# Performance work log

Hardware: AMD Instinct MI355X
Metric: run time of the kernel (lower is better)

Reference implementation:

```python
import jax, jax.numpy as jnp
import numpy as np

B, S, D_MODEL, N_HEADS, HIDDEN = 4, 2048, 1024, 16, 4096
D_HEAD = D_MODEL // N_HEADS
LN_EPS = 1e-5


def setup_inputs() -> dict:
    key = jax.random.key(0)
    ks = jax.random.split(key, 20)
    s = 0.02
    return {
        "X": jax.random.normal(ks[0], (B, S, D_MODEL), dtype=jnp.float32),
        # attention projections (stored [in, out]; y = x @ W + b)
        "Wq": jax.random.normal(ks[1], (D_MODEL, D_MODEL), dtype=jnp.float32) * s,
        "bq": jnp.zeros((D_MODEL,), jnp.float32),
        "Wk": jax.random.normal(ks[2], (D_MODEL, D_MODEL), dtype=jnp.float32) * s,
        "bk": jnp.zeros((D_MODEL,), jnp.float32),
        "Wv": jax.random.normal(ks[3], (D_MODEL, D_MODEL), dtype=jnp.float32) * s,
        "bv": jnp.zeros((D_MODEL,), jnp.float32),
        "Wo": jax.random.normal(ks[4], (D_MODEL, D_MODEL), dtype=jnp.float32) * s,
        "bo": jnp.zeros((D_MODEL,), jnp.float32),
        # layernorm 1
        "g1": jnp.ones((D_MODEL,), jnp.float32),
        "beta1": jnp.zeros((D_MODEL,), jnp.float32),
        # FFN
        "W1": jax.random.normal(ks[5], (D_MODEL, HIDDEN), dtype=jnp.float32) * s,
        "b1": jnp.zeros((HIDDEN,), jnp.float32),
        "W2": jax.random.normal(ks[6], (HIDDEN, D_MODEL), dtype=jnp.float32) * s,
        "b2": jnp.zeros((D_MODEL,), jnp.float32),
        # layernorm 2
        "g2": jnp.ones((D_MODEL,), jnp.float32),
        "beta2": jnp.zeros((D_MODEL,), jnp.float32),
    }


def _layer_norm(x, gamma, beta):
    mu = jnp.mean(x, axis=-1, keepdims=True)
    var = jnp.mean(jnp.square(x - mu), axis=-1, keepdims=True)
    return (x - mu) * jax.lax.rsqrt(var + LN_EPS) * gamma + beta


def reference(X, Wq, bq, Wk, bk, Wv, bv, Wo, bo, g1, beta1, W1, b1, W2, b2, g2, beta2):
    b, s, d = X.shape
    # multi-head attention (dropout is identity in eval mode)
    q = (X @ Wq + bq).reshape(b, s, N_HEADS, D_HEAD)
    k = (X @ Wk + bk).reshape(b, s, N_HEADS, D_HEAD)
    v = (X @ Wv + bv).reshape(b, s, N_HEADS, D_HEAD)
    scale = 1.0 / np.sqrt(D_HEAD).astype(np.float32)
    scores = jnp.einsum('bqhd,bkhd->bhqk', q, k) * scale
    attn = jax.nn.softmax(scores, axis=-1)
    ctx = jnp.einsum('bhqk,bkhd->bqhd', attn, v).reshape(b, s, d)
    attn_out = ctx @ Wo + bo
    # AddNorm 1
    Y = _layer_norm(X + attn_out, g1, beta1)
    # FFN
    ffn_out = jax.nn.relu(Y @ W1 + b1) @ W2 + b2
    # AddNorm 2
    return _layer_norm(Y + ffn_out, g2, beta2)
```

## Files before the change

### kernel.cpp

```cpp
#include <hip/hip_runtime.h>
#include <stdint.h>

typedef unsigned short u16;
typedef short bf16x8 __attribute__((ext_vector_type(8)));
typedef float f32x4 __attribute__((ext_vector_type(4)));
typedef float f32x16 __attribute__((ext_vector_type(16)));
typedef u16 u16x4 __attribute__((ext_vector_type(4)));
typedef u16 u16x8 __attribute__((ext_vector_type(8)));

#define LOG2E 1.4426950408889634f
#define QSCALE (0.125f * LOG2E)

__device__ __forceinline__ u16 f2bf(float f) {
  union { float f; uint32_t u; } x; x.f = f;
  uint32_t r = x.u + 0x7fffu + ((x.u >> 16) & 1u);
  return (u16)(r >> 16);
}
__device__ __forceinline__ u16 f2bf_ru(float f) {
  union { float f; uint32_t u; } x; x.f = f;
  return (u16)((x.u + 0x8000u) >> 16);
}
__device__ __forceinline__ float bf2f(u16 h) {
  union { uint32_t u; float f; } x; x.u = ((uint32_t)h) << 16;
  return x.f;
}
__device__ __forceinline__ uint32_t cvtpk(float lo, float hi) {
  uint32_t r;
  asm("v_cvt_pk_bf16_f32 %0, %1, %2" : "=v"(r) : "v"(lo), "v"(hi));
  return r;
}
__device__ __forceinline__ int swz3(int row) { return (row ^ (row >> 3)) & 7; }

__device__ __forceinline__ void gload_lds16(const void* g, void* lds) {
  __builtin_amdgcn_global_load_lds(
      (const __attribute__((address_space(1))) void*)g,
      (__attribute__((address_space(3))) void*)lds, 16, 0, 0);
}

__global__ __launch_bounds__(256) void cast_bf16(const float* __restrict__ in,
                                                 u16* __restrict__ out, int n8) {
  int i = blockIdx.x * 256 + threadIdx.x;
  const int stride = gridDim.x * 256;
  for (; i < n8; i += stride) {
    const f32x4* p = (const f32x4*)in + (size_t)i * 2;
    f32x4 a = p[0], b = p[1];
    u16x8 o;
    o[0] = f2bf(a[0]); o[1] = f2bf(a[1]); o[2] = f2bf(a[2]); o[3] = f2bf(a[3]);
    o[4] = f2bf(b[0]); o[5] = f2bf(b[1]); o[6] = f2bf(b[2]); o[7] = f2bf(b[3]);
    ((u16x8*)out)[i] = o;
  }
}

__global__ __launch_bounds__(256) void concat3(const float* __restrict__ a,
                                               const float* __restrict__ b,
                                               const float* __restrict__ c,
                                               float* __restrict__ o) {
  int i = blockIdx.x * 256 + threadIdx.x;
  if (i < 3072)
    o[i] = i < 1024 ? a[i] * QSCALE : (i < 2048 ? b[i - 1024] : c[i - 2048]);
}

__global__ __launch_bounds__(256) void transpose_cast(const float* __restrict__ in,
                                                      u16* __restrict__ out, int R, int C,
                                                      float scale) {
  __shared__ float tile[32][33];
  const int bc = blockIdx.x * 32, br = blockIdx.y * 32;
  const int tx = threadIdx.x & 31, ty = threadIdx.x >> 5;
#pragma unroll
  for (int i = 0; i < 32; i += 8)
    tile[ty + i][tx] = in[(size_t)(br + ty + i) * C + bc + tx];
  __syncthreads();
#pragma unroll
  for (int i = 0; i < 32; i += 8)
    out[(size_t)(bc + ty + i) * R + br + tx] = f2bf(tile[tx][ty + i] * scale);
}

__global__ __launch_bounds__(256) void vtrans(const u16* __restrict__ QKV,
                                              u16* __restrict__ Vtg) {
  __shared__ u16 tl[64][65];
  const int t = threadIdx.x;
  const int sblk = blockIdx.x, h = blockIdx.y, b = blockIdx.z;
  const int s0 = sblk * 64;
  const size_t ibase = ((size_t)b * 2048) * 3072 + 2048 + h * 64;
#pragma unroll
  for (int i = 0; i < 2; i++) {
    const int idx = i * 256 + t;
    const int sl = idx >> 3, d0 = (idx & 7) * 8;
    bf16x8 v = *(const bf16x8*)&QKV[ibase + (size_t)(s0 + sl) * 3072 + d0];
#pragma unroll
    for (int e = 0; e < 8; e++) tl[d0 + e][sl] = (u16)v[e];
  }
  __syncthreads();
  const size_t ob = ((size_t)(b * 16 + h) * 64) * 2048;
#pragma unroll
  for (int i = 0; i < 2; i++) {
    const int idx = i * 256 + t;
    const int r = idx >> 3, c0 = (idx & 7) * 8;
    u16x8 o;
#pragma unroll
    for (int e = 0; e < 8; e++) o[e] = tl[r][c0 + e];
    *(u16x8*)&Vtg[ob + (size_t)r * 2048 + s0 + c0] = o;
  }
}

template <int RELU>
__global__ __launch_bounds__(512, 2) void gemm8p(const u16* __restrict__ A,
                                                 const u16* __restrict__ BT,
                                                 const float* __restrict__ bias,
                                                 u16* __restrict__ Cb,
                                                 int M, int N, int K, int nbx) {
  __shared__ u16 As[2][256 * 64];
  __shared__ u16 Bs[2][256 * 64];
  const int t = threadIdx.x;
  const int w = t >> 6, lane = t & 63;
  const int l5 = lane & 31, hf = lane >> 5;
  const int wr = w >> 2, wc = w & 3;
  int bid = (int)blockIdx.x;
  const int cpx = (int)gridDim.x >> 3;
  bid = (bid & 7) * cpx + (bid >> 3);
  const int m0 = (bid / nbx) * 256, n0 = (bid % nbx) * 256;
  const int NT = K >> 6;
  const int row64 = t >> 3;
  const int colp = ((t & 7) ^ swz3(row64)) << 3;

#define STG_A(buf, tile, q) \
  gload_lds16(A + (size_t)(m0 + (q)*64 + row64) * K + ((tile) << 6) + colp, \
              &As[buf][(q)*4096 + w * 512])
#define STG_B(buf, tile, q) \
  gload_lds16(BT + (size_t)(n0 + (q)*64 + row64) * K + ((tile) << 6) + colp, \
              &Bs[buf][(q)*4096 + w * 512])
#define LDA32(dst, mfi, kb) { const int r_ = wr * 128 + (mfi)*32 + l5; \
  dst = *(const bf16x8*)&As[cur][r_ * 64 + (((((kb) << 1) + hf) ^ swz3(r_)) << 3)]; }
#define LDB32(dst, nfi, kb) { const int r_ = wc * 64 + (nfi)*32 + l5; \
  dst = *(const bf16x8*)&Bs[cur][r_ * 64 + (((((kb) << 1) + hf) ^ swz3(r_)) << 3)]; }
#define MFMA32(mh, nfi, barr) \
  __builtin_amdgcn_s_setprio(1); \
  _Pragma("unroll") for (int kb = 0; kb < 4; kb++) \
  _Pragma("unroll") for (int i = 0; i < 2; i++) \
    acc[((mh)*2 + i) * 2 + (nfi)] = __builtin_amdgcn_mfma_f32_32x32x16_bf16( \
        af[i][kb], barr[kb], acc[((mh)*2 + i) * 2 + (nfi)], 0, 0, 0); \
  __builtin_amdgcn_s_setprio(0);
#define BAR1() __builtin_amdgcn_s_barrier(); \
  asm volatile("s_waitcnt lgkmcnt(0)" ::: "memory"); \
  __builtin_amdgcn_sched_barrier(0)

  f32x16 acc[8];
#pragma unroll
  for (int i = 0; i < 8; i++)
#pragma unroll
    for (int j = 0; j < 16; j++) acc[i][j] = 0.f;

  STG_A(0, 0, 0); STG_A(0, 0, 2);
  STG_B(0, 0, 0); STG_B(0, 0, 1); STG_B(0, 0, 2); STG_B(0, 0, 3);
  STG_A(0, 0, 1); STG_A(0, 0, 3);
  asm volatile("s_waitcnt vmcnt(2)" ::: "memory");
  __builtin_amdgcn_s_barrier();

  for (int tile = 0; tile < NT; ++tile) {
    const int cur = tile & 1, nxt = cur ^ 1;
    const bool hn = (tile + 1) < NT;
    bf16x8 af[2][4], b0[4], b1[4];
#pragma unroll
    for (int kb = 0; kb < 4; kb++) { LDA32(af[0][kb], 0, kb); LDA32(af[1][kb], 1, kb); }
#pragma unroll
    for (int kb = 0; kb < 4; kb++) { LDB32(b0[kb], 0, kb); }
    if (hn) { STG_A(nxt, tile + 1, 0); STG_A(nxt, tile + 1, 2); }
    BAR1();
    MFMA32(0, 0, b0);
    __builtin_amdgcn_s_barrier();
#pragma unroll
    for (int kb = 0; kb < 4; kb++) { LDB32(b1[kb], 1, kb); }
    if (hn) { STG_B(nxt, tile + 1, 0); STG_B(nxt, tile + 1, 1); }
    BAR1();
    MFMA32(0, 1, b1);
    if (hn) { asm volatile("s_waitcnt vmcnt(4)" ::: "memory"); }
    else    { asm volatile("s_waitcnt vmcnt(0)" ::: "memory"); }
    __builtin_amdgcn_s_barrier();
#pragma unroll
    for (int kb = 0; kb < 4; kb++) { LDA32(af[0][kb], 2, kb); LDA32(af[1][kb], 3, kb); }
    if (hn) { STG_B(nxt, tile + 1, 2); STG_B(nxt, tile + 1, 3); }
    BAR1();
    MFMA32(1, 0, b0);
    __builtin_amdgcn_s_barrier();
    if (hn) { STG_A(nxt, tile + 1, 1); STG_A(nxt, tile + 1, 3); }
    BAR1();
    MFMA32(1, 1, b1);
    if (hn) { asm volatile("s_waitcnt vmcnt(2)" ::: "memory"); }
    __builtin_amdgcn_s_barrier();
  }
#undef STG_A
#undef STG_B
#undef LDA32
#undef LDB32
#undef MFMA32
#undef BAR1

#pragma unroll
  for (int mf = 0; mf < 4; mf++) {
#pragma unroll
    for (int nf = 0; nf < 2; nf++) {
      const int c = n0 + wc * 64 + nf * 32 + l5;
      const float bv = bias[c];
#pragma unroll
      for (int reg = 0; reg < 16; reg++) {
        const int r = m0 + wr * 128 + mf * 32 + (reg & 3) + 8 * (reg >> 2) + 4 * hf;
        float v = acc[mf * 2 + nf][reg] + bv;
        if (RELU) v = fmaxf(v, 0.f);
        Cb[(size_t)r * N + c] = f2bf(v);
      }
    }
  }
}

template <int RELU>
__global__ __launch_bounds__(512, 2) void gemm8n(const u16* __restrict__ A,
                                                 const u16* __restrict__ BT,
                                                 const float* __restrict__ bias,
                                                 u16* __restrict__ Cb,
                                                 int M, int N, int K, int nbx) {
  __shared__ u16 As[2][128 * 64];
  __shared__ u16 Bs[2][256 * 64];
  const int t = threadIdx.x;
  const int w = t >> 6, lane = t & 63;
  const int l5 = lane & 31, hf = lane >> 5;
  const int wr = w >> 2, wc = w & 3;
  int bid = (int)blockIdx.x;
  const int cpx = (int)gridDim.x >> 3;
  bid = (bid & 7) * cpx + (bid >> 3);
  const int m0 = (bid / nbx) * 128, n0 = (bid % nbx) * 256;
  const int NT = K >> 6;
  const int rowA = t >> 3;
  const int colpA = ((t & 7) ^ swz3(rowA)) << 3;

#define STG_An(buf, tile, q) \
  gload_lds16(A + (size_t)(m0 + (q)*64 + rowA) * K + ((tile) << 6) + colpA, \
              &As[buf][(q)*4096 + t * 8])
#define STG_Bn(buf, tile, c, i) { \
  const int r32_ = (i)*64 + (t >> 3); \
  const int R_ = ((r32_ >> 5) << 6) + (c)*32 + (r32_ & 31); \
  const int cp_ = ((t & 7) ^ swz3(R_)) << 3; \
  gload_lds16(BT + (size_t)(n0 + R_) * K + ((tile) << 6) + cp_, \
              &Bs[buf][R_ * 64 + (t & 7) * 8]); }
#define LDAn(dst, mfi, kb) { const int r_ = wr * 64 + (mfi)*32 + l5; \
  dst = *(const bf16x8*)&As[cur][r_ * 64 + (((((kb) << 1) + hf) ^ swz3(r_)) << 3)]; }
#define LDBn(dst, nfi, kb) { const int r_ = wc * 64 + (nfi)*32 + l5; \
  dst = *(const bf16x8*)&Bs[cur][r_ * 64 + (((((kb) << 1) + hf) ^ swz3(r_)) << 3)]; }
#define MFMAn(nfi, barr) \
  __builtin_amdgcn_s_setprio(1); \
  _Pragma("unroll") for (int kb = 0; kb < 4; kb++) \
  _Pragma("unroll") for (int i = 0; i < 2; i++) \
    acc[i * 2 + (nfi)] = __builtin_amdgcn_mfma_f32_32x32x16_bf16( \
        af[i][kb], barr[kb], acc[i * 2 + (nfi)], 0, 0, 0); \
  __builtin_amdgcn_s_setprio(0);
#define BARn() __builtin_amdgcn_s_barrier(); \
  asm volatile("s_waitcnt lgkmcnt(0)" ::: "memory"); \
  __builtin_amdgcn_sched_barrier(0)

  f32x16 acc[4];
#pragma unroll
  for (int i = 0; i < 4; i++)
#pragma unroll
    for (int j = 0; j < 16; j++) acc[i][j] = 0.f;

  STG_Bn(0, 0, 0, 0); STG_Bn(0, 0, 0, 1); STG_An(0, 0, 0);
  STG_An(0, 0, 1); STG_Bn(0, 0, 1, 0); STG_Bn(0, 0, 1, 1);
  asm volatile("s_waitcnt vmcnt(0)" ::: "memory");
  __builtin_amdgcn_s_barrier();

  for (int tile = 0; tile < NT; ++tile) {
    const int cur = tile & 1, nxt = cur ^ 1;
    const bool hn = (tile + 1) < NT;
    bf16x8 af[2][4], b0[4], b1[4];
#pragma unroll
    for (int kb = 0; kb < 4; kb++) { LDAn(af[0][kb], 0, kb); LDAn(af[1][kb], 1, kb); }
#pragma unroll
    for (int kb = 0; kb < 4; kb++) { LDBn(b0[kb], 0, kb); }
    if (hn) { STG_Bn(nxt, tile + 1, 0, 0); STG_Bn(nxt, tile + 1, 0, 1); STG_An(nxt, tile + 1, 0); }
    BARn();
    MFMAn(0, b0);
    if (hn) { asm volatile("s_waitcnt vmcnt(3)" ::: "memory"); }
    else    { asm volatile("s_waitcnt vmcnt(0)" ::: "memory"); }
    __builtin_amdgcn_s_barrier();
#pragma unroll
    for (int kb = 0; kb < 4; kb++) { LDBn(b1[kb], 1, kb); }
    if (hn) { STG_An(nxt, tile + 1, 1); STG_Bn(nxt, tile + 1, 1, 0); STG_Bn(nxt, tile + 1, 1, 1); }
    BARn();
    MFMAn(1, b1);
    if (hn) { asm volatile("s_waitcnt vmcnt(2)" ::: "memory"); }
    __builtin_amdgcn_s_barrier();
  }
#undef STG_An
#undef STG_Bn
#undef LDAn
#undef LDBn
#undef MFMAn
#undef BARn

#pragma unroll
  for (int mf = 0; mf < 2; mf++) {
#pragma unroll
    for (int nf = 0; nf < 2; nf++) {
      const int c = n0 + wc * 64 + nf * 32 + l5;
      const float bv = bias[c];
#pragma unroll
      for (int reg = 0; reg < 16; reg++) {
        const int r = m0 + wr * 64 + mf * 32 + (reg & 3) + 8 * (reg >> 2) + 4 * hf;
        float v = acc[mf * 2 + nf][reg] + bv;
        if (RELU) v = fmaxf(v, 0.f);
        Cb[(size_t)r * N + c] = f2bf(v);
      }
    }
  }
}

__global__ __launch_bounds__(256, 3) void attn_fwd(const u16* __restrict__ Qg,
                                                   const u16* __restrict__ Kg,
                                                   const u16* __restrict__ Vtg,
                                                   u16* __restrict__ Og, int LDM) {
  constexpr int S = 2048, DMO = 1024, NT = S / 64;
  __shared__ u16 Ks[2][64 * 64];
  __shared__ u16 Vt[2][64 * 64];
  const int t = threadIdx.x, w = t >> 6, lane = t & 63;
  const int l5 = lane & 31, hf = lane >> 5;
  const int qb = blockIdx.x, h = blockIdx.y, b = blockIdx.z;
  const size_t base = ((size_t)b * S) * LDM + h * 64;
  const size_t vbase = ((size_t)(b * 16 + h) * 64) * 2048;
  const size_t obase = ((size_t)b * S) * DMO + h * 64;
  const int qrow0 = qb * 128 + w * 32;

#define ATT_STAGE(buf, kt_) { \
  _Pragma("unroll") for (int i = 0; i < 2; i++) { \
    const int s = i * 256 + t; const int r = s >> 3; const int cg = s & 7; \
    gload_lds16(Kg + base + (size_t)((kt_) + r) * LDM + ((cg ^ swz3(r)) << 3), \
                &Ks[buf][s * 8]); } \
  _Pragma("unroll") for (int i = 0; i < 2; i++) { \
    const int s = i * 256 + t; const int r = s >> 3; const int cg = s & 7; \
    gload_lds16(Vtg + vbase + (size_t)r * 2048 + (kt_) + ((cg ^ swz3(r)) << 3), \
                &Vt[buf][s * 8]); } }

  bf16x8 qf[4];
#pragma unroll
  for (int kb = 0; kb < 4; kb++)
    qf[kb] = *(const bf16x8*)&Qg[base + (size_t)(qrow0 + l5) * LDM + kb * 16 + hf * 8];

  f32x16 accO0, accO1, accL;
#pragma unroll
  for (int i = 0; i < 16; i++) { accO0[i] = 0.f; accO1[i] = 0.f; accL[i] = 0.f; }
  float m = -1e30f;

  bf16x8 ones;
#pragma unroll
  for (int i = 0; i < 8; i++) ones[i] = (short)0x3F80;

  ATT_STAGE(0, 0);
  asm volatile("s_waitcnt vmcnt(0)" ::: "memory");
  __builtin_amdgcn_s_barrier();

  for (int kt = 0; kt < NT; ++kt) {
    const int cur = kt & 1;
    if (kt + 1 < NT) ATT_STAGE(cur ^ 1, (kt + 1) * 64);

    f32x16 st0, st1;
#pragma unroll
    for (int i = 0; i < 16; i++) { st0[i] = 0.f; st1[i] = 0.f; }
    __builtin_amdgcn_s_setprio(1);
#pragma unroll
    for (int kb = 0; kb < 4; kb++) {
      const int r0 = l5, r1 = 32 + l5;
      bf16x8 kf0 = *(const bf16x8*)&Ks[cur][r0 * 64 + (((hf + 2 * kb) ^ swz3(r0)) << 3)];
      bf16x8 kf1 = *(const bf16x8*)&Ks[cur][r1 * 64 + (((hf + 2 * kb) ^ swz3(r1)) << 3)];
      st0 = __builtin_amdgcn_mfma_f32_32x32x16_bf16(kf0, qf[kb], st0, 0, 0, 0);
      st1 = __builtin_amdgcn_mfma_f32_32x32x16_bf16(kf1, qf[kb], st1, 0, 0, 0);
    }
    __builtin_amdgcn_s_setprio(0);

    float rm = st0[0];
#pragma unroll
    for (int i = 1; i < 16; i++) rm = fmaxf(rm, st0[i]);
#pragma unroll
    for (int i = 0; i < 16; i++) rm = fmaxf(rm, st1[i]);
    if (__any(rm > m + 8.0f)) {
      float ra = rm, rb = rm;
      asm volatile("v_permlane32_swap_b32 %0, %1" : "+v"(ra), "+v"(rb));
      rm = fmaxf(rm, fmaxf(ra, rb));
      const float mN = fmaxf(m, rm);
      const float al = exp2f(m - mN);
      m = mN;
#pragma unroll
      for (int r = 0; r < 16; r++) {
        const float alr = __shfl(al, (r & 3) + 8 * (r >> 2) + 4 * hf, 64);
        accO0[r] *= alr; accO1[r] *= alr; accL[r] *= alr;
      }
    }

    uint32_t pw0[8], pw1[8];
#pragma unroll
    for (int r2 = 0; r2 < 8; r2++) {
      pw0[r2] = cvtpk(exp2f(st0[2 * r2] - m), exp2f(st0[2 * r2 + 1] - m));
      pw1[r2] = cvtpk(exp2f(st1[2 * r2] - m), exp2f(st1[2 * r2 + 1] - m));
    }
    bf16x8 pf[4];
    {
      uint32_t a0 = pw0[0], b0v = pw0[2], a1 = pw0[1], b1v = pw0[3];
      asm volatile("v_permlane32_swap_b32 %0, %1" : "+v"(a0), "+v"(b0v));
      asm volatile("v_permlane32_swap_b32 %0, %1" : "+v"(a1), "+v"(b1v));
      union { uint32_t u[4]; bf16x8 v; } k;
      k.u[0] = a0; k.u[1] = a1; k.u[2] = b0v; k.u[3] = b1v; pf[0] = k.v;
      uint32_t c0 = pw0[4], d0 = pw0[6], c1 = pw0[5], d1 = pw0[7];
      asm volatile("v_permlane32_swap_b32 %0, %1" : "+v"(c0), "+v"(d0));
      asm volatile("v_permlane32_swap_b32 %0, %1" : "+v"(c1), "+v"(d1));
      k.u[0] = c0; k.u[1] = c1; k.u[2] = d0; k.u[3] = d1; pf[1] = k.v;
      uint32_t e0 = pw1[0], f0 = pw1[2], e1 = pw1[1], f1 = pw1[3];
      asm volatile("v_permlane32_swap_b32 %0, %1" : "+v"(e0), "+v"(f0));
      asm volatile("v_permlane32_swap_b32 %0, %1" : "+v"(e1), "+v"(f1));
      k.u[0] = e0; k.u[1] = e1; k.u[2] = f0; k.u[3] = f1; pf[2] = k.v;
      uint32_t g0 = pw1[4], h0 = pw1[6], g1 = pw1[5], h1 = pw1[7];
      asm volatile("v_permlane32_swap_b32 %0, %1" : "+v"(g0), "+v"(h0));
      asm volatile("v_permlane32_swap_b32 %0, %1" : "+v"(g1), "+v"(h1));
      k.u[0] = g0; k.u[1] = g1; k.u[2] = h0; k.u[3] = h1; pf[3] = k.v;
    }

    __builtin_amdgcn_s_setprio(1);
#pragma unroll
    for (int kb = 0; kb < 4; kb++) {
      const int r0 = l5, r1 = 32 + l5;
      bf16x8 vf0 = *(const bf16x8*)&Vt[cur][r0 * 64 + (((hf + 2 * kb) ^ swz3(r0)) << 3)];
      bf16x8 vf1 = *(const bf16x8*)&Vt[cur][r1 * 64 + (((hf + 2 * kb) ^ swz3(r1)) << 3)];
      accO0 = __builtin_amdgcn_mfma_f32_32x32x16_bf16(pf[kb], vf0, accO0, 0, 0, 0);
      accO1 = __builtin_amdgcn_mfma_f32_32x32x16_bf16(pf[kb], vf1, accO1, 0, 0, 0);
      accL  = __builtin_amdgcn_mfma_f32_32x32x16_bf16(pf[kb], ones, accL, 0, 0, 0);
    }
    __builtin_amdgcn_s_setprio(0);

    asm volatile("s_waitcnt vmcnt(0)" ::: "memory");
    __builtin_amdgcn_s_barrier();
  }
#undef ATT_STAGE

#pragma unroll
  for (int r = 0; r < 16; r++) {
    const float inv = 1.0f / accL[r];
    const int row = qrow0 + (r & 3) + 8 * (r >> 2) + 4 * hf;
    Og[obase + (size_t)row * DMO + l5]      = f2bf_ru(accO0[r] * inv);
    Og[obase + (size_t)row * DMO + 32 + l5] = f2bf_ru(accO1[r] * inv);
  }
}

template <int AF32, int OUTF32>
__global__ __launch_bounds__(256) void add_ln(const void* __restrict__ Ap,
                                              const u16* __restrict__ Bb,
                                              const float* __restrict__ g,
                                              const float* __restrict__ be,
                                              void* __restrict__ Yp) {
  constexpr int D = 1024;
  const int row = blockIdx.x, t = threadIdx.x;
  f32x4 a;
  if (AF32) {
    a = ((const f32x4*)((const float*)Ap + (size_t)row * D))[t];
  } else {
    u16x4 av = ((const u16x4*)((const u16*)Ap + (size_t)row * D))[t];
#pragma unroll
    for (int i = 0; i < 4; i++) a[i] = bf2f(av[i]);
  }
  u16x4 bv16 = ((const u16x4*)(Bb + (size_t)row * D))[t];
  f32x4 x;
#pragma unroll
  for (int i = 0; i < 4; i++) x[i] = a[i] + bf2f(bv16[i]);
  float s1 = x[0] + x[1] + x[2] + x[3];
  float s2 = x[0] * x[0] + x[1] * x[1] + x[2] * x[2] + x[3] * x[3];
#pragma unroll
  for (int off = 32; off > 0; off >>= 1) {
    s1 += __shfl_down(s1, off, 64);
    s2 += __shfl_down(s2, off, 64);
  }
  __shared__ float sm[8];
  const int w = t >> 6, lane = t & 63;
  if (lane == 0) { sm[w] = s1; sm[4 + w] = s2; }
  __syncthreads();
  s1 = sm[0] + sm[1] + sm[2] + sm[3];
  s2 = sm[4] + sm[5] + sm[6] + sm[7];
  const float mean = s1 * (1.0f / D);
  const float var = s2 * (1.0f / D) - mean * mean;
  const float rstd = rsqrtf(var + 1e-5f);
  const f32x4 gv = ((const f32x4*)g)[t];
  const f32x4 bv = ((const f32x4*)be)[t];
  f32x4 y;
#pragma unroll
  for (int i = 0; i < 4; i++) y[i] = (x[i] - mean) * rstd * gv[i] + bv[i];
  if (OUTF32) {
    ((f32x4*)((float*)Yp + (size_t)row * D))[t] = y;
  } else {
    u16x4 o;
#pragma unroll
    for (int i = 0; i < 4; i++) o[i] = f2bf(y[i]);
    ((u16x4*)((u16*)Yp + (size_t)row * D))[t] = o;
  }
}

extern "C" void kernel_launch(void* const* d_in, const int* in_sizes, int n_in,
                              void* d_out, int out_size, void* d_ws, size_t ws_size,
                              hipStream_t stream) {
  const float* X   = (const float*)d_in[0];
  const float* Wq  = (const float*)d_in[1];
  const float* bq  = (const float*)d_in[2];
  const float* Wk  = (const float*)d_in[3];
  const float* bk  = (const float*)d_in[4];
  const float* Wv  = (const float*)d_in[5];
  const float* bv  = (const float*)d_in[6];
  const float* Wo  = (const float*)d_in[7];
  const float* bo  = (const float*)d_in[8];
  const float* g1  = (const float*)d_in[9];
  const float* be1 = (const float*)d_in[10];
  const float* W1  = (const float*)d_in[11];
  const float* b1  = (const float*)d_in[12];
  const float* W2  = (const float*)d_in[13];
  const float* b2  = (const float*)d_in[14];
  const float* g2  = (const float*)d_in[15];
  const float* be2 = (const float*)d_in[16];

  const size_t MB = 1ull << 20;
  char* wsb = (char*)d_ws;
  u16*   WqkvT = (u16*)(wsb + 0 * MB);
  u16*   WoT   = (u16*)(wsb + 6 * MB);
  u16*   W1T   = (u16*)(wsb + 8 * MB);
  u16*   W2T   = (u16*)(wsb + 16 * MB);
  u16*   Xb    = (u16*)(wsb + 24 * MB);
  u16*   Ab    = (u16*)(wsb + 24 * MB);
  u16*   Fb    = (u16*)(wsb + 24 * MB);
  u16*   QKVb  = (u16*)(wsb + 40 * MB);
  u16*   Hb    = (u16*)(wsb + 40 * MB);
  float* bqkv  = (float*)(wsb + 88 * MB);
  u16*   Cx    = (u16*)(wsb + 88 * MB);
  u16*   Vt_g  = (u16*)(wsb + 104 * MB);
  u16*   Yb    = (u16*)(wsb + 104 * MB);
  (void)ws_size; (void)in_sizes; (void)n_in; (void)out_size;

  cast_bf16<<<2048, 256, 0, stream>>>(X, Xb, 8192 * 1024 / 8);
  concat3<<<12, 256, 0, stream>>>(bq, bk, bv, bqkv);
  transpose_cast<<<dim3(32, 32), 256, 0, stream>>>(Wq, WqkvT, 1024, 1024, QSCALE);
  transpose_cast<<<dim3(32, 32), 256, 0, stream>>>(Wk, WqkvT + 1024 * 1024, 1024, 1024, 1.0f);
  transpose_cast<<<dim3(32, 32), 256, 0, stream>>>(Wv, WqkvT + 2 * 1024 * 1024, 1024, 1024, 1.0f);
  transpose_cast<<<dim3(32, 32), 256, 0, stream>>>(Wo, WoT, 1024, 1024, 1.0f);
  transpose_cast<<<dim3(128, 32), 256, 0, stream>>>(W1, W1T, 1024, 4096, 1.0f);
  transpose_cast<<<dim3(32, 128), 256, 0, stream>>>(W2, W2T, 4096, 1024, 1.0f);

  gemm8p<0><<<384, 512, 0, stream>>>(Xb, WqkvT, bqkv, QKVb, 8192, 3072, 1024, 12);

  vtrans<<<dim3(32, 16, 4), 256, 0, stream>>>(QKVb, Vt_g);
  attn_fwd<<<dim3(16, 16, 4), 256, 0, stream>>>(QKVb, QKVb + 1024, Vt_g, Cx, 3072);

  gemm8n<0><<<256, 512, 0, stream>>>(Cx, WoT, bo, Ab, 8192, 1024, 1024, 4);
  add_ln<1, 0><<<8192, 256, 0, stream>>>(X, Ab, g1, be1, Yb);
  gemm8p<1><<<512, 512, 0, stream>>>(Yb, W1T, b1, Hb, 8192, 4096, 1024, 16);
  gemm8n<0><<<256, 512, 0, stream>>>(Hb, W2T, b2, Fb, 8192, 1024, 4096, 4);
  add_ln<0, 1><<<8192, 256, 0, stream>>>(Yb, Fb, g2, be2, d_out);
}
```

Baseline: 415.3 us.

## Merge prep kernels into one launch and fuse V transpose into QKV GEMM epilogue

Replaces the separate cast, bias-concat and six weight transpose launches with a single prep kernel that dispatches by block index. The QKV GEMM epilogue now also writes the transposed V layout directly, so the standalone vtrans kernel is removed. This cuts launch overhead and one read/write pass over V. In exchange the GEMM epilogue does extra scattered 8-byte stores for the V columns.

After: 402.7 us. 1.03x faster.

```diff
diff --git a/kernel.cpp b/kernel.cpp
--- a/kernel.cpp
+++ b/kernel.cpp
@@ -37,77 +37,57 @@
       (__attribute__((address_space(3))) void*)lds, 16, 0, 0);
 }
 
-__global__ __launch_bounds__(256) void cast_bf16(const float* __restrict__ in,
-                                                 u16* __restrict__ out, int n8) {
-  int i = blockIdx.x * 256 + threadIdx.x;
-  const int stride = gridDim.x * 256;
-  for (; i < n8; i += stride) {
-    const f32x4* p = (const f32x4*)in + (size_t)i * 2;
-    f32x4 a = p[0], b = p[1];
-    u16x8 o;
-    o[0] = f2bf(a[0]); o[1] = f2bf(a[1]); o[2] = f2bf(a[2]); o[3] = f2bf(a[3]);
-    o[4] = f2bf(b[0]); o[5] = f2bf(b[1]); o[6] = f2bf(b[2]); o[7] = f2bf(b[3]);
-    ((u16x8*)out)[i] = o;
-  }
-}
-
-__global__ __launch_bounds__(256) void concat3(const float* __restrict__ a,
-                                               const float* __restrict__ b,
-                                               const float* __restrict__ c,
-                                               float* __restrict__ o) {
-  int i = blockIdx.x * 256 + threadIdx.x;
-  if (i < 3072)
-    o[i] = i < 1024 ? a[i] * QSCALE : (i < 2048 ? b[i - 1024] : c[i - 2048]);
-}
-
-__global__ __launch_bounds__(256) void transpose_cast(const float* __restrict__ in,
-                                                      u16* __restrict__ out, int R, int C,
-                                                      float scale) {
-  __shared__ float tile[32][33];
-  const int bc = blockIdx.x * 32, br = blockIdx.y * 32;
-  const int tx = threadIdx.x & 31, ty = threadIdx.x >> 5;
-#pragma unroll
-  for (int i = 0; i < 32; i += 8)
-    tile[ty + i][tx] = in[(size_t)(br + ty + i) * C + bc + tx];
-  __syncthreads();
-#pragma unroll
-  for (int i = 0; i < 32; i += 8)
-    out[(size_t)(bc + ty + i) * R + br + tx] = f2bf(tile[tx][ty + i] * scale);
-}
-
-__global__ __launch_bounds__(256) void vtrans(const u16* __restrict__ QKV,
-                                              u16* __restrict__ Vtg) {
-  __shared__ u16 tl[64][65];
-  const int t = threadIdx.x;
-  const int sblk = blockIdx.x, h = blockIdx.y, b = blockIdx.z;
-  const int s0 = sblk * 64;
-  const size_t ibase = ((size_t)b * 2048) * 3072 + 2048 + h * 64;
-#pragma unroll
-  for (int i = 0; i < 2; i++) {
-    const int idx = i * 256 + t;
-    const int sl = idx >> 3, d0 = (idx & 7) * 8;
-    bf16x8 v = *(const bf16x8*)&QKV[ibase + (size_t)(s0 + sl) * 3072 + d0];
-#pragma unroll
-    for (int e = 0; e < 8; e++) tl[d0 + e][sl] = (u16)v[e];
-  }
-  __syncthreads();
-  const size_t ob = ((size_t)(b * 16 + h) * 64) * 2048;
-#pragma unroll
-  for (int i = 0; i < 2; i++) {
-    const int idx = i * 256 + t;
-    const int r = idx >> 3, c0 = (idx & 7) * 8;
-    u16x8 o;
-#pragma unroll
-    for (int e = 0; e < 8; e++) o[e] = tl[r][c0 + e];
-    *(u16x8*)&Vtg[ob + (size_t)r * 2048 + s0 + c0] = o;
-  }
-}
-
-template <int RELU>
+__global__ __launch_bounds__(256) void prep(
+    const float* __restrict__ X, u16* __restrict__ Xb,
+    const float* __restrict__ Wq, const float* __restrict__ Wk,
+    const float* __restrict__ Wv, const float* __restrict__ Wo,
+    const float* __restrict__ W1, const float* __restrict__ W2,
+    u16* __restrict__ WqkvT, u16* __restrict__ WoT,
+    u16* __restrict__ W1T, u16* __restrict__ W2T,
+    const float* __restrict__ bq, const float* __restrict__ bk,
+    const float* __restrict__ bv, float* __restrict__ bqkv) {
+  const int blk = blockIdx.x, t = threadIdx.x;
+  if (blk < 2048) {
+    const int n8 = 8192 * 1024 / 8;
+    for (int i = blk * 256 + t; i < n8; i += 2048 * 256) {
+      const f32x4* p = (const f32x4*)X + (size_t)i * 2;
+      f32x4 a = p[0], b = p[1];
+      u16x8 o;
+      o[0] = f2bf(a[0]); o[1] = f2bf(a[1]); o[2] = f2bf(a[2]); o[3] = f2bf(a[3]);
+      o[4] = f2bf(b[0]); o[5] = f2bf(b[1]); o[6] = f2bf(b[2]); o[7] = f2bf(b[3]);
+      ((u16x8*)Xb)[i] = o;
+    }
+  } else if (blk < 14336) {
+    const float* tin; u16* tout; int R, C; float sc; int bx, by;
+    if (blk < 3072)      { tin = Wq; tout = WqkvT;                R = 1024; C = 1024; sc = QSCALE; bx = (blk - 2048) & 31;  by = (blk - 2048) >> 5; }
+    else if (blk < 4096) { tin = Wk; tout = WqkvT + 1024 * 1024;  R = 1024; C = 1024; sc = 1.f;    bx = (blk - 3072) & 31;  by = (blk - 3072) >> 5; }
+    else if (blk < 5120) { tin = Wv; tout = WqkvT + 2 * 1024 * 1024; R = 1024; C = 1024; sc = 1.f; bx = (blk - 4096) & 31;  by = (blk - 4096) >> 5; }
+    else if (blk < 6144) { tin = Wo; tout = WoT;                  R = 1024; C = 1024; sc = 1.f;    bx = (blk - 5120) & 31;  by = (blk - 5120) >> 5; }
+    else if (blk < 10240){ tin = W1; tout = W1T;                  R = 1024; C = 4096; sc = 1.f;    bx = (blk - 6144) & 127; by = (blk - 6144) >> 7; }
+    else                 { tin = W2; tout = W2T;                  R = 4096; C = 1024; sc = 1.f;    bx = (blk - 10240) & 31; by = (blk - 10240) >> 5; }
+    __shared__ float tile[32][33];
+    const int bc = bx * 32, br = by * 32;
+    const int tx = t & 31, ty = t >> 5;
+#pragma unroll
+    for (int i = 0; i < 32; i += 8)
+      tile[ty + i][tx] = tin[(size_t)(br + ty + i) * C + bc + tx];
+    __syncthreads();
+#pragma unroll
+    for (int i = 0; i < 32; i += 8)
+      tout[(size_t)(bc + ty + i) * R + br + tx] = f2bf(tile[tx][ty + i] * sc);
+  } else {
+    const int i = (blk - 14336) * 256 + t;
+    if (i < 3072)
+      bqkv[i] = i < 1024 ? bq[i] * QSCALE : (i < 2048 ? bk[i - 1024] : bv[i - 2048]);
+  }
+}
+
+template <int RELU, int VDUAL>
 __global__ __launch_bounds__(512, 2) void gemm8p(const u16* __restrict__ A,
                                                  const u16* __restrict__ BT,
                                                  const float* __restrict__ bias,
                                                  u16* __restrict__ Cb,
+                                                 u16* __restrict__ Vtg,
                                                  int M, int N, int K, int nbx) {
   __shared__ u16 As[2][256 * 64];
   __shared__ u16 Bs[2][256 * 64];
@@ -201,12 +181,26 @@
     for (int nf = 0; nf < 2; nf++) {
       const int c = n0 + wc * 64 + nf * 32 + l5;
       const float bv = bias[c];
+      u16 vals[16];
 #pragma unroll
       for (int reg = 0; reg < 16; reg++) {
         const int r = m0 + wr * 128 + mf * 32 + (reg & 3) + 8 * (reg >> 2) + 4 * hf;
         float v = acc[mf * 2 + nf][reg] + bv;
         if (RELU) v = fmaxf(v, 0.f);
-        Cb[(size_t)r * N + c] = f2bf(v);
+        vals[reg] = f2bf(v);
+        Cb[(size_t)r * N + c] = vals[reg];
+      }
+      if (VDUAL && n0 >= 2048) {
+        const int h = (c - 2048) >> 6, dh = (c - 2048) & 63;
+#pragma unroll
+        for (int rg = 0; rg < 4; rg++) {
+          const int r0 = m0 + wr * 128 + mf * 32 + rg * 8 + 4 * hf;
+          const int b = r0 >> 11, s = r0 & 2047;
+          u16x4 o;
+#pragma unroll
+          for (int e = 0; e < 4; e++) o[e] = vals[rg * 4 + e];
+          *(u16x4*)&Vtg[((size_t)(b * 16 + h) * 64 + dh) * 2048 + s] = o;
+        }
       }
     }
   }
@@ -535,23 +529,16 @@
   u16*   Yb    = (u16*)(wsb + 104 * MB);
   (void)ws_size; (void)in_sizes; (void)n_in; (void)out_size;
 
-  cast_bf16<<<2048, 256, 0, stream>>>(X, Xb, 8192 * 1024 / 8);
-  concat3<<<12, 256, 0, stream>>>(bq, bk, bv, bqkv);
-  transpose_cast<<<dim3(32, 32), 256, 0, stream>>>(Wq, WqkvT, 1024, 1024, QSCALE);
-  transpose_cast<<<dim3(32, 32), 256, 0, stream>>>(Wk, WqkvT + 1024 * 1024, 1024, 1024, 1.0f);
-  transpose_cast<<<dim3(32, 32), 256, 0, stream>>>(Wv, WqkvT + 2 * 1024 * 1024, 1024, 1024, 1.0f);
-  transpose_cast<<<dim3(32, 32), 256, 0, stream>>>(Wo, WoT, 1024, 1024, 1.0f);
-  transpose_cast<<<dim3(128, 32), 256, 0, stream>>>(W1, W1T, 1024, 4096, 1.0f);
-  transpose_cast<<<dim3(32, 128), 256, 0, stream>>>(W2, W2T, 4096, 1024, 1.0f);
-
-  gemm8p<0><<<384, 512, 0, stream>>>(Xb, WqkvT, bqkv, QKVb, 8192, 3072, 1024, 12);
-
-  vtrans<<<dim3(32, 16, 4), 256, 0, stream>>>(QKVb, Vt_g);
+  prep<<<14348, 256, 0, stream>>>(X, Xb, Wq, Wk, Wv, Wo, W1, W2,
+                                  WqkvT, WoT, W1T, W2T, bq, bk, bv, bqkv);
+
+  gemm8p<0, 1><<<384, 512, 0, stream>>>(Xb, WqkvT, bqkv, QKVb, Vt_g, 8192, 3072, 1024, 12);
+
   attn_fwd<<<dim3(16, 16, 4), 256, 0, stream>>>(QKVb, QKVb + 1024, Vt_g, Cx, 3072);
 
   gemm8n<0><<<256, 512, 0, stream>>>(Cx, WoT, bo, Ab, 8192, 1024, 1024, 4);
   add_ln<1, 0><<<8192, 256, 0, stream>>>(X, Ab, g1, be1, Yb);
-  gemm8p<1><<<512, 512, 0, stream>>>(Yb, W1T, b1, Hb, 8192, 4096, 1024, 16);
+  gemm8p<1, 0><<<512, 512, 0, stream>>>(Yb, W1T, b1, Hb, nullptr, 8192, 4096, 1024, 16);
   gemm8n<0><<<256, 512, 0, stream>>>(Hb, W2T, b2, Fb, 8192, 1024, 4096, 4);
   add_ln<0, 1><<<8192, 256, 0, stream>>>(Yb, Fb, g2, be2, d_out);
 }
```
